# Optimization experiments

Hardware: AMD Instinct MI355X
Metric: run time of the kernel (lower is better)

## Reference

```python
import math
import jax, jax.numpy as jnp
import numpy as np

B, S, D = 4, 2048, 1024
NEG = -1e20

def setup_inputs() -> dict:
    key = jax.random.key(0)
    k1, k2, k3, k4 = jax.random.split(key, 4)
    X = jax.random.normal(k1, (B, S, D), dtype=jnp.float32)
    # True = masked position (masked_fill semantics)
    attention_mask = jax.random.randint(k2, (B, S, S), 0, 2).astype(bool)
    scale = 1.0 / math.sqrt(D)
    W_qkv = jax.random.normal(k3, (D, 3 * D), dtype=jnp.float32) * scale
    b_qkv = jnp.zeros((3 * D,), dtype=jnp.float32)
    W_out = jax.random.normal(k4, (D, D), dtype=jnp.float32) * scale
    b_out = jnp.zeros((D,), dtype=jnp.float32)
    return {"X": X, "attention_mask": attention_mask,
            "W_qkv": W_qkv, "b_qkv": b_qkv, "W_out": W_out, "b_out": b_out}

def reference(X, attention_mask, W_qkv, b_qkv, W_out, b_out):
    dim = X.shape[-1]
    QKV = X @ W_qkv + b_qkv                      # [B,S,3D]
    Q, K, V = jnp.split(QKV, 3, axis=-1)         # each [B,S,D]
    scores = jnp.einsum('bqd,bkd->bqk', Q, K) / math.sqrt(dim)  # [B,S,S]
    scores = jnp.where(attention_mask, NEG, scores)
    attn = jax.nn.softmax(scores, axis=-1)       # dropout_rate=0.0 -> identity
    ctx = jnp.einsum('bqk,bkd->bqd', attn, V)    # [B,S,D]
    return ctx @ W_out + b_out
```

## Files before the change

### kernel.cpp

```cpp
#include <hip/hip_runtime.h>
#include <cstdint>
#include <cstddef>

#define BB 4
#define SS 2048
#define DD 1024

typedef _Float16 f16;
typedef _Float16 f16x8 __attribute__((ext_vector_type(8)));
typedef _Float16 f16x4 __attribute__((ext_vector_type(4)));
typedef float fx4 __attribute__((ext_vector_type(4)));

__device__ __forceinline__ void async_copy16(void* lds, const void* g) {
  __builtin_amdgcn_global_load_lds(
      (__attribute__((address_space(1))) void*)const_cast<void*>(g),
      (__attribute__((address_space(3))) void*)lds,
      16, 0, 0);
}

enum { EPI_BIAS = 0, EPI_MASKEXP = 1, EPI_ROWSCALE = 2, EPI_QKV = 3 };

template <typename OutT, int MODE>
__global__ __launch_bounds__(256, 2) void gemm_nt(
    const f16* __restrict__ A, long long strideA, int lda,
    const f16* __restrict__ Bt, long long strideB, int ldb,
    OutT* __restrict__ C, long long strideC, int ldc,
    const float* __restrict__ bias, const uint32_t* __restrict__ gmask,
    float* __restrict__ rowSum, f16* __restrict__ vt, float scale, int K) {
  __shared__ __align__(16) char smem[49152];

  const int t = threadIdx.x;
  const int lane = t & 63;
  const int wid = t >> 6;
  const long long bz = blockIdx.z;
  const int tileM = blockIdx.y * 128;
  const int tileN = blockIdx.x * 128;

  const f16* Ab = A + bz * strideA;
  const f16* Bb = Bt + bz * strideB;
  OutT* Cb = C + bz * strideC;

  const int sr = t >> 2;
  const int sc = (((t & 3) ^ ((t >> 3) & 3)) * 8);
  const f16* pa0 = Ab + (size_t)(tileM + sr) * lda + sc;
  const f16* pa1 = Ab + (size_t)(tileM + 64 + sr) * lda + sc;
  const f16* pb0 = Bb + (size_t)(tileN + sr) * ldb + sc;
  const f16* pb1 = Bb + (size_t)(tileN + 64 + sr) * ldb + sc;
  const int tb = t * 16;

  const int waveM = (wid >> 1) * 64;
  const int waveN = (wid & 1) * 64;
  const int r16 = lane & 15;
  const int quad = lane >> 4;
  const int sw = (r16 >> 1) & 3;

  const int nIter = K >> 5;

#define STG(buf, kk)                              \
  {                                               \
    char* nb_ = smem + (buf) * 16384;             \
    async_copy16(nb_ + tb, pa0 + (kk));           \
    async_copy16(nb_ + 4096 + tb, pa1 + (kk));    \
    async_copy16(nb_ + 8192 + tb, pb0 + (kk));    \
    async_copy16(nb_ + 12288 + tb, pb1 + (kk));   \
  }

  STG(0, 0);
  STG(1, 32);

  fx4 acc[4][4] = {};

#pragma unroll 3
  for (int i = 0; i < nIter; ++i) {
    if (i + 1 < nIter) {
      asm volatile("s_waitcnt vmcnt(4)" ::: "memory");
    } else {
      asm volatile("s_waitcnt vmcnt(0)" ::: "memory");
    }
    __builtin_amdgcn_s_barrier();
    __builtin_amdgcn_sched_barrier(0);
    if (i + 2 < nIter) STG((i + 2) % 3, (i + 2) << 5);

    const f16* As = (const f16*)(smem + (i % 3) * 16384);
    const f16* Bs = As + 4096;

    f16x8 af[4], bf[4];
#pragma unroll
    for (int x = 0; x < 4; ++x)
      af[x] = *(const f16x8*)&As[(waveM + x * 16 + r16) * 32 + (quad ^ sw) * 8];
#pragma unroll
    for (int x = 0; x < 4; ++x)
      bf[x] = *(const f16x8*)&Bs[(waveN + x * 16 + r16) * 32 + (quad ^ sw) * 8];

#pragma unroll
    for (int x = 0; x < 4; ++x)
#pragma unroll
      for (int j = 0; j < 4; ++j)
        acc[x][j] =
            __builtin_amdgcn_mfma_f32_16x16x32_f16(af[x], bf[j], acc[x][j], 0, 0, 0);
  }
#undef STG

  if constexpr (MODE == EPI_BIAS) {
#pragma unroll
    for (int j = 0; j < 4; ++j) {
      const int col = tileN + waveN + j * 16 + r16;
      const float bv = bias[col];
#pragma unroll
      for (int i = 0; i < 4; ++i) {
#pragma unroll
        for (int r = 0; r < 4; ++r) {
          const int row = tileM + waveM + i * 16 + quad * 4 + r;
          Cb[(size_t)row * ldc + col] = (OutT)(acc[i][j][r] * scale + bv);
        }
      }
    }
  } else if constexpr (MODE == EPI_QKV) {
    if (tileN < 2 * DD) {
#pragma unroll
      for (int j = 0; j < 4; ++j) {
        const int col = tileN + waveN + j * 16 + r16;
        const float bv = bias[col];
#pragma unroll
        for (int i = 0; i < 4; ++i) {
#pragma unroll
          for (int r = 0; r < 4; ++r) {
            const int row = tileM + waveM + i * 16 + quad * 4 + r;
            Cb[(size_t)row * ldc + col] = (OutT)(acc[i][j][r] + bv);
          }
        }
      }
    } else {
      const int b = tileM >> 11;
      const int s0 = (tileM & 2047) + waveM;
      f16* vb = vt + (size_t)b * DD * SS;
#pragma unroll
      for (int j = 0; j < 4; ++j) {
        const int col = tileN + waveN + j * 16 + r16;
        const float bv = bias[col];
        const int d = col - 2 * DD;
#pragma unroll
        for (int i = 0; i < 4; ++i) {
          const int s = s0 + i * 16 + quad * 4;
          f16x4 v4;
#pragma unroll
          for (int r = 0; r < 4; ++r) v4[r] = (f16)(acc[i][j][r] + bv);
          *(f16x4*)&vb[(size_t)d * SS + s] = v4;
        }
      }
    }
  } else if constexpr (MODE == EPI_MASKEXP) {
#pragma unroll
    for (int i = 0; i < 4; ++i) {
#pragma unroll
      for (int r = 0; r < 4; ++r) {
        const int row = tileM + waveM + i * 16 + quad * 4 + r;
        const uint32_t* gr =
            gmask + (((size_t)bz * SS + row) << 6) + ((tileN + waveN) >> 5);
        const uint32_t w0 = gr[0], w1 = gr[1];
        float part = 0.0f;
#pragma unroll
        for (int j = 0; j < 4; ++j) {
          const int bitpos = j * 16 + r16;
          const uint32_t mv = ((j < 2 ? w0 : w1) >> (bitpos & 31)) & 1u;
          const float e = mv ? 0.0f : __expf(acc[i][j][r] * scale);
          Cb[(size_t)row * ldc + tileN + waveN + j * 16 + r16] = (OutT)e;
          part += e;
        }
#pragma unroll
        for (int d = 1; d < 16; d <<= 1) part += __shfl_xor(part, d, 64);
        if (r16 == 0) atomicAdd(&rowSum[bz * SS + row], part);
      }
    }
  } else {
#pragma unroll
    for (int i = 0; i < 4; ++i) {
#pragma unroll
      for (int r = 0; r < 4; ++r) {
        const int row = tileM + waveM + i * 16 + quad * 4 + r;
        const float inv = scale / rowSum[bz * SS + row];
#pragma unroll
        for (int j = 0; j < 4; ++j) {
          const int col = tileN + waveN + j * 16 + r16;
          Cb[(size_t)row * ldc + col] = (OutT)(acc[i][j][r] * inv);
        }
      }
    }
  }
}

__global__ __launch_bounds__(256) void k_prep(
    const float* __restrict__ X, f16* __restrict__ Xh,
    const float* __restrict__ Wqkv, f16* __restrict__ Wqkvt,
    const float* __restrict__ Wout, f16* __restrict__ Woutt,
    float* __restrict__ rowSum, const int* __restrict__ mask,
    uint32_t* __restrict__ gmask) {
  int bid = blockIdx.x;
  const int t = threadIdx.x;
  if (bid < 8192) {
    const int i = bid * 256 + t;
    const float4 v = ((const float4*)X)[i];
    f16x4 h = {(f16)v.x, (f16)v.y, (f16)v.z, (f16)v.w};
    ((f16x4*)Xh)[i] = h;
    return;
  }
  bid -= 8192;
  __shared__ float tile[32][33];
  const int tx = t & 31, ty = t >> 5;
  if (bid < 3072) {
    const int bx = (bid % 96) * 32, by = (bid / 96) * 32;
    for (int i2 = ty; i2 < 32; i2 += 8)
      tile[i2][tx] = Wqkv[(size_t)(by + i2) * 3072 + bx + tx];
    __syncthreads();
    for (int i2 = ty; i2 < 32; i2 += 8)
      Wqkvt[(size_t)(bx + i2) * 1024 + by + tx] = (f16)tile[tx][i2];
    return;
  }
  bid -= 3072;
  if (bid < 1024) {
    const int bx = (bid & 31) * 32, by = (bid >> 5) * 32;
    for (int i2 = ty; i2 < 32; i2 += 8)
      tile[i2][tx] = Wout[(size_t)(by + i2) * 1024 + bx + tx];
    __syncthreads();
    for (int i2 = ty; i2 < 32; i2 += 8)
      Woutt[(size_t)(bx + i2) * 1024 + by + tx] = (f16)tile[tx][i2];
    return;
  }
  bid -= 1024;
  if (bid < 32) {
    rowSum[bid * 256 + t] = 0.0f;
    return;
  }
  bid -= 32;
  const int w = bid * 256 + t;
  const int4* mr = (const int4*)(mask + ((size_t)w << 5));
  uint32_t v = 0;
#pragma unroll
  for (int c = 0; c < 8; ++c) {
    const int4 q = mr[c];
    v |= (q.x ? 1u : 0u) << (c * 4);
    v |= (q.y ? 1u : 0u) << (c * 4 + 1);
    v |= (q.z ? 1u : 0u) << (c * 4 + 2);
    v |= (q.w ? 1u : 0u) << (c * 4 + 3);
  }
  gmask[w] = v;
}

extern "C" void kernel_launch(void* const* d_in, const int* in_sizes, int n_in,
                              void* d_out, int out_size, void* d_ws, size_t ws_size,
                              hipStream_t stream) {
  const float* X = (const float*)d_in[0];
  const int* mask = (const int*)d_in[1];
  const float* Wqkv = (const float*)d_in[2];
  const float* bqkv = (const float*)d_in[3];
  const float* Wout = (const float*)d_in[4];
  const float* bout = (const float*)d_in[5];
  float* out = (float*)d_out;

  char* ws = (char*)d_ws;
  f16* Xh = (f16*)(ws + 0);
  f16* Wqkvt = (f16*)(ws + 16777216);
  f16* Woutt = (f16*)(ws + 23068672);
  f16* QK = (f16*)(ws + 25165824);
  f16* Vt = (f16*)(ws + 58720256);
  f16* E = (f16*)(ws + 75497472);
  f16* Ctx = (f16*)(ws + 109051904);
  float* rowSum = (float*)(ws + 125829120);
  uint32_t* gmask = (uint32_t*)(ws + 109051904);

  k_prep<<<dim3(14368), dim3(256), 0, stream>>>(X, Xh, Wqkv, Wqkvt, Wout, Woutt,
                                                rowSum, mask, gmask);

  gemm_nt<f16, EPI_QKV><<<dim3(24, 64, 1), dim3(256), 0, stream>>>(
      Xh, 0LL, DD, Wqkvt, 0LL, DD, QK, 0LL, 2 * DD, bqkv, nullptr, nullptr, Vt,
      1.0f, DD);

  gemm_nt<f16, EPI_MASKEXP><<<dim3(16, 16, 4), dim3(256), 0, stream>>>(
      QK, (long long)SS * 2 * DD, 2 * DD, QK + DD, (long long)SS * 2 * DD, 2 * DD,
      E, (long long)SS * SS, SS, nullptr, gmask, rowSum, nullptr, 0.03125f, DD);

  gemm_nt<f16, EPI_ROWSCALE><<<dim3(8, 16, 4), dim3(256), 0, stream>>>(
      E, (long long)SS * SS, SS, Vt, (long long)DD * SS, SS, Ctx,
      (long long)SS * DD, DD, nullptr, nullptr, rowSum, nullptr, 1.0f, SS);

  gemm_nt<float, EPI_BIAS><<<dim3(8, 64, 1), dim3(256), 0, stream>>>(
      Ctx, 0LL, DD, Woutt, 0LL, DD, out, 0LL, DD, bout, nullptr, nullptr, nullptr,
      1.0f, DD);
}
```

Baseline: 347.5 us.

## Switch GEMM to two-stage LDS buffering and remap tiles across XCDs

Reduces the GEMM shared-memory pipeline from three stages (48KB) to two (32KB). The hand-placed partial vmcnt waits are replaced by a plain __syncthreads followed by one prefetch per iteration. Block indices are also remapped so consecutive tiles are spread in chunks across the 8 XCDs, aiming for better L2 reuse. The two-stage scheme leaves less time to hide load latency and drains all loads at each barrier. The remap assumes the tile count is divisible by 8.

```diff
diff --git a/kernel.cpp b/kernel.cpp
--- a/kernel.cpp
+++ b/kernel.cpp
@@ -27,14 +27,19 @@
     OutT* __restrict__ C, long long strideC, int ldc,
     const float* __restrict__ bias, const uint32_t* __restrict__ gmask,
     float* __restrict__ rowSum, f16* __restrict__ vt, float scale, int K) {
-  __shared__ __align__(16) char smem[49152];
+  __shared__ __align__(16) char smem[32768];
 
   const int t = threadIdx.x;
   const int lane = t & 63;
   const int wid = t >> 6;
   const long long bz = blockIdx.z;
-  const int tileM = blockIdx.y * 128;
-  const int tileN = blockIdx.x * 128;
+
+  const int nxy = gridDim.x * gridDim.y;
+  const int bxy = blockIdx.y * gridDim.x + blockIdx.x;
+  const int chunk = nxy >> 3;
+  const int wk = (bxy & 7) * chunk + (bxy >> 3);
+  const int tileN = (wk % gridDim.x) * 128;
+  const int tileM = (wk / gridDim.x) * 128;
 
   const f16* Ab = A + bz * strideA;
   const f16* Bb = Bt + bz * strideB;
@@ -55,33 +60,28 @@
   const int sw = (r16 >> 1) & 3;
 
   const int nIter = K >> 5;
-
-#define STG(buf, kk)                              \
-  {                                               \
-    char* nb_ = smem + (buf) * 16384;             \
-    async_copy16(nb_ + tb, pa0 + (kk));           \
-    async_copy16(nb_ + 4096 + tb, pa1 + (kk));    \
-    async_copy16(nb_ + 8192 + tb, pb0 + (kk));    \
-    async_copy16(nb_ + 12288 + tb, pb1 + (kk));   \
-  }
-
-  STG(0, 0);
-  STG(1, 32);
+  {
+    char* b0 = smem;
+    async_copy16(b0 + tb, pa0);
+    async_copy16(b0 + 4096 + tb, pa1);
+    async_copy16(b0 + 8192 + tb, pb0);
+    async_copy16(b0 + 12288 + tb, pb1);
+  }
 
   fx4 acc[4][4] = {};
 
-#pragma unroll 3
+#pragma unroll 2
   for (int i = 0; i < nIter; ++i) {
+    __syncthreads();
     if (i + 1 < nIter) {
-      asm volatile("s_waitcnt vmcnt(4)" ::: "memory");
-    } else {
-      asm volatile("s_waitcnt vmcnt(0)" ::: "memory");
-    }
-    __builtin_amdgcn_s_barrier();
-    __builtin_amdgcn_sched_barrier(0);
-    if (i + 2 < nIter) STG((i + 2) % 3, (i + 2) << 5);
-
-    const f16* As = (const f16*)(smem + (i % 3) * 16384);
+      char* nb = smem + ((i + 1) & 1) * 16384;
+      const int k = (i + 1) << 5;
+      async_copy16(nb + tb, pa0 + k);
+      async_copy16(nb + 4096 + tb, pa1 + k);
+      async_copy16(nb + 8192 + tb, pb0 + k);
+      async_copy16(nb + 12288 + tb, pb1 + k);
+    }
+    const f16* As = (const f16*)(smem + (i & 1) * 16384);
     const f16* Bs = As + 4096;
 
     f16x8 af[4], bf[4];
@@ -99,7 +99,6 @@
         acc[x][j] =
             __builtin_amdgcn_mfma_f32_16x16x32_f16(af[x], bf[j], acc[x][j], 0, 0, 0);
   }
-#undef STG
 
   if constexpr (MODE == EPI_BIAS) {
 #pragma unroll
```

New measurement: 342.3 us. No clear change (-1.5%).
